# Kernel tuning notes

Measured on AMD Instinct MI355X. Metric: run time of the kernel, lower is better.

## Reference

```python
import jax, jax.numpy as jnp
import numpy as np

N_ITEMS = 100000
N_USERS = 40000
EMB = 100
NNZ_A = 3200000
NNZ_U = 1600000
BATCH = 4096
LAYERS = 3


def setup_inputs() -> dict:
    key = jax.random.key(0)
    ks = jax.random.split(key, 9)
    return {
        "adj_vals": jax.random.uniform(ks[0], (NNZ_A,), dtype=jnp.float32),
        "u_vals": jax.random.uniform(ks[1], (NNZ_U,), dtype=jnp.float32),
        "embedding": jax.random.normal(ks[2], (N_ITEMS, EMB), dtype=jnp.float32),
        "user_embedding": jax.random.normal(ks[3], (N_USERS, EMB), dtype=jnp.float32),
        "adj_rows": jax.random.randint(ks[4], (NNZ_A,), 0, N_ITEMS),
        "adj_cols": jax.random.randint(ks[5], (NNZ_A,), 0, N_ITEMS),
        "u_rows": jax.random.randint(ks[6], (NNZ_U,), 0, N_USERS),
        "u_cols": jax.random.randint(ks[7], (NNZ_U,), 0, N_ITEMS),
        "user": jax.random.randint(ks[8], (BATCH,), 0, N_USERS),
    }


def spmm(vals, rows, cols, x, n_rows):
    # COO sparse (n_rows x n_cols) @ dense x: gather rows of x by col index,
    # scale by nnz values, scatter-add into output rows.
    return jax.ops.segment_sum(vals[:, None] * x[cols], rows, num_segments=n_rows)


def reference(adj_vals, u_vals, embedding, user_embedding,
              adj_rows, adj_cols, u_rows, u_cols, user):
    # Multi-hop hypergraph propagation with running layer-sum (final = sum of layers 0..L)
    x = embedding
    total = x
    for _ in range(LAYERS):
        x = spmm(adj_vals, adj_rows, adj_cols, x, embedding.shape[0])
        total = total + x
    # ishyper branch: user embeddings = (u_adj @ summed item embeddings)[user]
    user_all = spmm(u_vals, u_rows, u_cols, total, user_embedding.shape[0])
    return total, user_all[user]
```

## Files before the change

kernel.cpp:

```cpp
#include <hip/hip_runtime.h>
#include <stdint.h>

#define EMB 100
#define HW 50
#define HW2 25
#define V4_PER_ROW 25
#define BSHIFT 8
#define NBMAX 1024
#define TP 256
#define EP 32

#define SCAN_T 256
#define SCAN_E 32

static __device__ __forceinline__ uint32_t pack_bf16(float a, float b) {
    uint32_t ua = __float_as_uint(a);
    uint32_t ub = __float_as_uint(b);
    ua = (ua + 0x7FFFu + ((ua >> 16) & 1u)) >> 16;
    ub = (ub + 0x7FFFu + ((ub >> 16) & 1u)) >> 16;
    return ua | (ub << 16);
}
static __device__ __forceinline__ float bflo(uint32_t p) { return __uint_as_float(p << 16); }
static __device__ __forceinline__ float bfhi(uint32_t p) { return __uint_as_float(p & 0xFFFF0000u); }

__global__ void convert_bf16(const float2* __restrict__ x, uint32_t* __restrict__ xbf, int nwords) {
    for (int i = blockIdx.x * blockDim.x + threadIdx.x; i < nwords; i += gridDim.x * blockDim.x) {
        float2 v = x[i];
        xbf[i] = pack_bf16(v.x, v.y);
    }
}

__global__ void map_build(const int* __restrict__ user, uint32_t* __restrict__ map, int batch) {
    int i = blockIdx.x * blockDim.x + threadIdx.x;
    if (i < batch) atomicMin(&map[user[i]], (uint32_t)i);
}

__global__ __launch_bounds__(TP) void pass1_count(
    const int* __restrict__ ra, int na, const int* __restrict__ ru, int nu,
    const uint32_t* __restrict__ map, int* __restrict__ countsT,
    int nblk, int nbA, int nbTot)
{
    __shared__ int lc[NBMAX];
    const int blk = blockIdx.x;
    for (int i = threadIdx.x; i < nbTot; i += TP) lc[i] = 0;
    __syncthreads();
    const int base = blk * (TP * EP);
    const int n = na + nu;
    for (int i = 0; i < EP; ++i) {
        int e = base + i * TP + threadIdx.x;
        int b = -1;
        if (e < na) {
            b = __builtin_nontemporal_load(ra + e) >> BSHIFT;
        } else if (e < n) {
            int r = __builtin_nontemporal_load(ru + (e - na));
            if (map[r] != 0xFFFFFFFFu) b = nbA + (r >> BSHIFT);
        }
        if (b >= 0) atomicAdd(&lc[b], 1);
    }
    __syncthreads();
    for (int i = threadIdx.x; i < nbTot; i += TP)
        countsT[(size_t)i * nblk + blk] = lc[i];
}

__global__ void scan_blocks(const int* __restrict__ in, int* __restrict__ out,
                            int* __restrict__ sums, int n) {
    __shared__ int smem[SCAN_T];
    const int b = blockIdx.x, tid = threadIdx.x;
    const int base = b * SCAN_T * SCAN_E + tid * SCAN_E;
    int loc[SCAN_E];
    int s = 0;
    for (int i = 0; i < SCAN_E; ++i) {
        int idx = base + i;
        int v = (idx < n) ? in[idx] : 0;
        loc[i] = s; s += v;
    }
    smem[tid] = s; __syncthreads();
    for (int off = 1; off < SCAN_T; off <<= 1) {
        int v = (tid >= off) ? smem[tid - off] : 0;
        __syncthreads();
        smem[tid] += v;
        __syncthreads();
    }
    int pre = (tid == 0) ? 0 : smem[tid - 1];
    if (tid == SCAN_T - 1) sums[b] = smem[tid];
    for (int i = 0; i < SCAN_E; ++i) {
        int idx = base + i;
        if (idx < n) out[idx] = pre + loc[i];
    }
}

__global__ void scan_mid(int* __restrict__ sums, int nb, int* __restrict__ total_out) {
    __shared__ int sh[256];
    const int t = threadIdx.x;
    int v = (t < nb) ? sums[t] : 0;
    sh[t] = v; __syncthreads();
    for (int off = 1; off < 256; off <<= 1) {
        int u = (t >= off) ? sh[t - off] : 0;
        __syncthreads();
        sh[t] += u;
        __syncthreads();
    }
    if (t < nb) sums[t] = sh[t];
    if (t == 255) *total_out = sh[255];
}

__global__ void scan_fixup(int* __restrict__ out, const int* __restrict__ sums, int n) {
    const int b = blockIdx.x;
    if (b == 0) return;
    const int add = sums[b - 1];
    const int base = b * SCAN_T * SCAN_E + threadIdx.x * SCAN_E;
    for (int i = 0; i < SCAN_E; ++i) {
        int idx = base + i;
        if (idx < n) out[idx] += add;
    }
}

__global__ void extract_bases(const int* __restrict__ scanned, int nblk, int nbTot,
                              const int* __restrict__ total, int* __restrict__ bases,
                              int* __restrict__ rpA_end, int nnzA, int* __restrict__ rpU_end) {
    int t = blockIdx.x * blockDim.x + threadIdx.x;
    if (t < nbTot) bases[t] = scanned[(size_t)t * nblk];
    if (t == 0) {
        int tot = *total;
        bases[nbTot] = tot;
        *rpA_end = nnzA;
        *rpU_end = tot - nnzA;
    }
}

__global__ __launch_bounds__(TP) void pass2_scatter(
    const float* __restrict__ va, const int* __restrict__ ra, const int* __restrict__ ia, int na,
    const float* __restrict__ vu, const int* __restrict__ ru, const int* __restrict__ iu, int nu,
    const uint32_t* __restrict__ map, const int* __restrict__ scanned,
    uint2* __restrict__ tmp, int nblk, int nbA, int nbTot)
{
    __shared__ int cur[NBMAX];
    const int blk = blockIdx.x;
    for (int i = threadIdx.x; i < nbTot; i += TP)
        cur[i] = scanned[(size_t)i * nblk + blk];
    __syncthreads();
    const int base = blk * (TP * EP);
    const int n = na + nu;
    for (int i = 0; i < EP; ++i) {
        int e = base + i * TP + threadIdx.x;
        if (e < na) {
            int r = __builtin_nontemporal_load(ra + e);
            int p = atomicAdd(&cur[r >> BSHIFT], 1);
            uint32_t key = ((uint32_t)(r & 255) << 17) | (uint32_t)__builtin_nontemporal_load(ia + e);
            tmp[p] = make_uint2(key, (uint32_t)__float_as_uint(__builtin_nontemporal_load(va + e)));
        } else if (e < n) {
            int k = e - na;
            int r = __builtin_nontemporal_load(ru + k);
            if (map[r] == 0xFFFFFFFFu) continue;
            int p = atomicAdd(&cur[nbA + (r >> BSHIFT)], 1);
            uint32_t key = ((uint32_t)(r & 255) << 17) | (uint32_t)__builtin_nontemporal_load(iu + k);
            tmp[p] = make_uint2(key, (uint32_t)__float_as_uint(__builtin_nontemporal_load(vu + k)));
        }
    }
}

__global__ __launch_bounds__(1024) void bucket_sort(const uint2* __restrict__ tmp,
                                                    const int* __restrict__ bases,
                                                    uint32_t* __restrict__ pk,
                                                    int* __restrict__ rpA, int* __restrict__ rpU,
                                                    int nbA, int nnzA, int nItems, int nUsers) {
    __shared__ int h[256];
    __shared__ int cur[256];
    const int t = threadIdx.x;
    const int b = blockIdx.x;
    const int lo = bases[b], hi = bases[b + 1];
    const bool isU = (b >= nbA);
    const int rowbase = (isU ? (b - nbA) : b) << BSHIFT;

    if (t < 256) h[t] = 0;
    __syncthreads();
    for (int i = lo + t; i < hi; i += 1024)
        atomicAdd(&h[tmp[i].x >> 17], 1);
    __syncthreads();
    int cnt = (t < 256) ? h[t] : 0;
    for (int off = 1; off < 256; off <<= 1) {
        int u = (t < 256 && t >= off) ? h[t - off] : 0;
        __syncthreads();
        if (t < 256) h[t] += u;
        __syncthreads();
    }
    if (t < 256) {
        int gpos = lo + h[t] - cnt;
        int row = rowbase + t;
        if (isU) { if (row < nUsers) rpU[row] = gpos - nnzA; }
        else     { if (row < nItems) rpA[row] = gpos; }
        cur[t] = gpos;
    }
    __syncthreads();
    for (int i = lo + t; i < hi; i += 1024) {
        uint2 e = tmp[i];
        int rl = (int)(e.x >> 17);
        uint32_t col = e.x & 0x1FFFFu;
        int p = atomicAdd(&cur[rl], 1);
        float v = __uint_as_float(e.y);
        uint32_t q = (uint32_t)(v * 32767.0f + 0.5f);
        if (q > 32767u) q = 32767u;
        pk[p] = (col << 15) | q;
    }
}

#define DECODE(w, v, c) { v = (float)((w) & 0x7FFFu) * (1.0f/32767.0f); c = (int)((w) >> 15); }

#define FMA2(vv, pp) { a0 = fmaf((vv), bflo((pp).x), a0); a1 = fmaf((vv), bfhi((pp).x), a1); \
                       a2 = fmaf((vv), bflo((pp).y), a2); a3 = fmaf((vv), bfhi((pp).y), a3); }

__global__ __launch_bounds__(256) void spmm_pk(
    const uint32_t* __restrict__ pk, const int* __restrict__ rowptr,
    const uint2* __restrict__ xbf2, uint2* __restrict__ outbf2,
    const float4* __restrict__ emb4, const uint2* __restrict__ x1bf2,
    const uint2* __restrict__ x2bf2, float4* __restrict__ total4,
    uint2* __restrict__ totbf2, int nrows)
{
    const int wid = (blockIdx.x * blockDim.x + threadIdx.x) >> 6;
    const int lane = threadIdx.x & 63;
    if (wid >= nrows) return;
    const int half = lane >> 5;
    const int l = lane & 31;
    const int start = rowptr[wid], end = rowptr[wid + 1];
    float a0 = 0.f, a1 = 0.f, a2 = 0.f, a3 = 0.f;
    for (int base = start; base < end; base += 64) {
        const int nc = min(64, end - base);
        uint32_t w = 0;
        if (lane < nc) w = __builtin_nontemporal_load(pk + base + lane);
        float myv; int myc;
        DECODE(w, myv, myc);
        int t = 0;
        for (; t + 8 <= nc; t += 8) {
            float v0 = __shfl(myv, t + half),     v1 = __shfl(myv, t + 2 + half);
            float v2 = __shfl(myv, t + 4 + half), v3 = __shfl(myv, t + 6 + half);
            int   c0 = __shfl(myc, t + half),     c1 = __shfl(myc, t + 2 + half);
            int   c2 = __shfl(myc, t + 4 + half), c3 = __shfl(myc, t + 6 + half);
            uint2 p0 = make_uint2(0u,0u), p1 = make_uint2(0u,0u);
            uint2 p2 = make_uint2(0u,0u), p3 = make_uint2(0u,0u);
            if (l < HW2) {
                p0 = xbf2[(size_t)c0 * HW2 + l];
                p1 = xbf2[(size_t)c1 * HW2 + l];
                p2 = xbf2[(size_t)c2 * HW2 + l];
                p3 = xbf2[(size_t)c3 * HW2 + l];
            }
            FMA2(v0, p0); FMA2(v1, p1); FMA2(v2, p2); FMA2(v3, p3);
        }
        for (; t < nc; t += 2) {
            int tt = min(t + half, nc - 1);
            float v0 = __shfl(myv, tt);
            int   c0 = __shfl(myc, tt);
            if (t + half >= nc) v0 = 0.f;
            uint2 p0 = make_uint2(0u,0u);
            if (l < HW2) p0 = xbf2[(size_t)c0 * HW2 + l];
            FMA2(v0, p0);
        }
    }
    a0 += __shfl_xor(a0, 32); a1 += __shfl_xor(a1, 32);
    a2 += __shfl_xor(a2, 32); a3 += __shfl_xor(a3, 32);
    if (lane < HW2) {
        const size_t widx = (size_t)wid * HW2 + lane;
        if (outbf2) {
            outbf2[widx] = make_uint2(pack_bf16(a0, a1), pack_bf16(a2, a3));
        } else {
            float4 e = emb4[widx];
            uint2 w1 = x1bf2[widx], w2 = x2bf2[widx];
            float t0 = e.x + bflo(w1.x) + bflo(w2.x) + a0;
            float t1 = e.y + bfhi(w1.x) + bfhi(w2.x) + a1;
            float t2 = e.z + bflo(w1.y) + bflo(w2.y) + a2;
            float t3 = e.w + bfhi(w1.y) + bfhi(w2.y) + a3;
            total4[widx] = make_float4(t0, t1, t2, t3);
            totbf2[widx] = make_uint2(pack_bf16(t0, t1), pack_bf16(t2, t3));
        }
    }
}

__global__ __launch_bounds__(256) void spmm_batch_pk(
    const uint32_t* __restrict__ pk, const int* __restrict__ rowptr,
    const int* __restrict__ user, const uint2* __restrict__ xbf2,
    float4* __restrict__ out4, int batch)
{
    const int wid = (blockIdx.x * blockDim.x + threadIdx.x) >> 6;
    const int lane = threadIdx.x & 63;
    if (wid >= batch) return;
    const int half = lane >> 5;
    const int l = lane & 31;
    const int row = user[wid];
    const int start = rowptr[row], end = rowptr[row + 1];
    float a0 = 0.f, a1 = 0.f, a2 = 0.f, a3 = 0.f;
    for (int base = start; base < end; base += 64) {
        const int nc = min(64, end - base);
        uint32_t w = 0;
        if (lane < nc) w = __builtin_nontemporal_load(pk + base + lane);
        float myv; int myc;
        DECODE(w, myv, myc);
        int t = 0;
        for (; t + 8 <= nc; t += 8) {
            float v0 = __shfl(myv, t + half),     v1 = __shfl(myv, t + 2 + half);
            float v2 = __shfl(myv, t + 4 + half), v3 = __shfl(myv, t + 6 + half);
            int   c0 = __shfl(myc, t + half),     c1 = __shfl(myc, t + 2 + half);
            int   c2 = __shfl(myc, t + 4 + half), c3 = __shfl(myc, t + 6 + half);
            uint2 p0 = make_uint2(0u,0u), p1 = make_uint2(0u,0u);
            uint2 p2 = make_uint2(0u,0u), p3 = make_uint2(0u,0u);
            if (l < HW2) {
                p0 = xbf2[(size_t)c0 * HW2 + l];
                p1 = xbf2[(size_t)c1 * HW2 + l];
                p2 = xbf2[(size_t)c2 * HW2 + l];
                p3 = xbf2[(size_t)c3 * HW2 + l];
            }
            FMA2(v0, p0); FMA2(v1, p1); FMA2(v2, p2); FMA2(v3, p3);
        }
        for (; t < nc; t += 2) {
            int tt = min(t + half, nc - 1);
            float v0 = __shfl(myv, tt);
            int   c0 = __shfl(myc, tt);
            if (t + half >= nc) v0 = 0.f;
            uint2 p0 = make_uint2(0u,0u);
            if (l < HW2) p0 = xbf2[(size_t)c0 * HW2 + l];
            FMA2(v0, p0);
        }
    }
    a0 += __shfl_xor(a0, 32); a1 += __shfl_xor(a1, 32);
    a2 += __shfl_xor(a2, 32); a3 += __shfl_xor(a3, 32);
    if (lane < HW2) out4[(size_t)wid * HW2 + lane] = make_float4(a0, a1, a2, a3);
}

__global__ void spmm_scatter(const float* __restrict__ vals, const int* __restrict__ rows,
                             const int* __restrict__ cols, const float* __restrict__ x,
                             float* __restrict__ out, int nnz) {
    long long t = (long long)blockIdx.x * blockDim.x + threadIdx.x;
    int e = (int)(t / V4_PER_ROW);
    int c = (int)(t % V4_PER_ROW);
    if (e >= nnz) return;
    int col = cols[e]; int row = rows[e]; float v = vals[e];
    const float4 g = *(const float4*)(x + (size_t)col * EMB + c * 4);
    float* o = out + (size_t)row * EMB + c * 4;
    atomicAdd(o + 0, v * g.x); atomicAdd(o + 1, v * g.y);
    atomicAdd(o + 2, v * g.z); atomicAdd(o + 3, v * g.w);
}
__global__ void add_inplace(float* __restrict__ acc, const float* __restrict__ x, int n4) {
    int i = blockIdx.x * blockDim.x + threadIdx.x;
    if (i < n4) {
        float4 a = ((const float4*)acc)[i];
        const float4 b = ((const float4*)x)[i];
        a.x += b.x; a.y += b.y; a.z += b.z; a.w += b.w;
        ((float4*)acc)[i] = a;
    }
}
__global__ void gather_rows(const float* __restrict__ src, const int* __restrict__ idx,
                            float* __restrict__ out, int nrows) {
    int t = blockIdx.x * blockDim.x + threadIdx.x;
    int r = t / V4_PER_ROW, c = t % V4_PER_ROW;
    if (r >= nrows) return;
    int s = idx[r];
    *(float4*)(out + (size_t)r * EMB + c * 4) = *(const float4*)(src + (size_t)s * EMB + c * 4);
}

static inline size_t align256(size_t x) { return (x + 255) & ~(size_t)255; }

extern "C" void kernel_launch(void* const* d_in, const int* in_sizes, int n_in,
                              void* d_out, int out_size, void* d_ws, size_t ws_size,
                              hipStream_t stream) {
    const float* adj_vals  = (const float*)d_in[0];
    const float* u_vals    = (const float*)d_in[1];
    const float* embedding = (const float*)d_in[2];
    const int*   adj_rows  = (const int*)d_in[4];
    const int*   adj_cols  = (const int*)d_in[5];
    const int*   u_rows    = (const int*)d_in[6];
    const int*   u_cols    = (const int*)d_in[7];
    const int*   user      = (const int*)d_in[8];

    const int NNZ_A   = in_sizes[0];
    const int NNZ_U   = in_sizes[1];
    const int N_ITEMS = in_sizes[2] / EMB;
    const int N_USERS = in_sizes[3] / EMB;
    const int BATCH   = in_sizes[8];

    const int NB_A = (N_ITEMS + 255) >> BSHIFT;
    const int NB_U = (N_USERS + 255) >> BSHIFT;
    const int NB_TOT = NB_A + NB_U;

    const int NNZ_T = NNZ_A + NNZ_U;
    const int nblk = (NNZ_T + TP * EP - 1) / (TP * EP);
    const long long nScan = (long long)NB_TOT * nblk;
    const int nsb = (int)((nScan + SCAN_T * SCAN_E - 1) / (SCAN_T * SCAN_E));

    float* total    = (float*)d_out;
    float* out_user = total + (size_t)N_ITEMS * EMB;

    const size_t rowWords = (size_t)N_ITEMS * HW;

    size_t off = 0;
    char* ws = (char*)d_ws;
    #define WS_ALLOC(name, bytes) char* name = ws + off; off += align256(bytes)
    WS_ALLOC(p_r0,      2 * rowWords * 4);
    WS_ALLOC(p_ebf,     rowWords * 4);
    WS_ALLOC(p_pk,      (size_t)NNZ_T * 4);
    WS_ALLOC(p_rpA,     ((size_t)N_ITEMS + 1) * 4);
    WS_ALLOC(p_rpU,     ((size_t)N_USERS + 1) * 4);
    WS_ALLOC(p_map,     (size_t)N_USERS * 4);
    WS_ALLOC(p_countsT, (size_t)nScan * 4);
    WS_ALLOC(p_sums,    256 * 4);
    WS_ALLOC(p_total,   4);
    WS_ALLOC(p_bases,   ((size_t)NB_TOT + 1) * 4);
    #undef WS_ALLOC
    const size_t tmpBytes = (size_t)NNZ_T * 8;

    if (ws_size >= off && tmpBytes <= 2 * rowWords * 4 && NB_TOT <= NBMAX && nsb <= 256
        && N_ITEMS <= (1 << 17) && N_USERS <= (1 << 17)) {
        uint32_t* x1bf  = (uint32_t*)p_r0;
        uint32_t* x2bf  = (uint32_t*)(p_r0 + rowWords * 4);
        uint2*    tmp   = (uint2*)p_r0;
        uint32_t* embbf = (uint32_t*)p_ebf;
        uint32_t* totbf = (uint32_t*)p_ebf;
        uint32_t* pk    = (uint32_t*)p_pk;
        int* rpA = (int*)p_rpA;
        int* rpU = (int*)p_rpU;
        uint32_t* map = (uint32_t*)p_map;
        int* countsT = (int*)p_countsT;
        int* sums    = (int*)p_sums;
        int* totalN  = (int*)p_total;
        int* bases   = (int*)p_bases;

        hipMemsetAsync(map, 0xFF, (size_t)N_USERS * 4, stream);
        map_build<<<(BATCH + 255) / 256, 256, 0, stream>>>(user, map, BATCH);

        convert_bf16<<<2048, 256, 0, stream>>>((const float2*)embedding, embbf, (int)rowWords);

        pass1_count<<<nblk, TP, 0, stream>>>(adj_rows, NNZ_A, u_rows, NNZ_U, map,
                                             countsT, nblk, NB_A, NB_TOT);
        scan_blocks<<<nsb, SCAN_T, 0, stream>>>(countsT, countsT, sums, (int)nScan);
        scan_mid<<<1, 256, 0, stream>>>(sums, nsb, totalN);
        scan_fixup<<<nsb, SCAN_T, 0, stream>>>(countsT, sums, (int)nScan);
        extract_bases<<<(NB_TOT + 255) / 256, 256, 0, stream>>>(countsT, nblk, NB_TOT, totalN,
                                                                bases, rpA + N_ITEMS, NNZ_A,
                                                                rpU + N_USERS);
        pass2_scatter<<<nblk, TP, 0, stream>>>(adj_vals, adj_rows, adj_cols, NNZ_A,
                                               u_vals, u_rows, u_cols, NNZ_U,
                                               map, countsT, tmp, nblk, NB_A, NB_TOT);
        bucket_sort<<<NB_TOT, 1024, 0, stream>>>(tmp, bases, pk, rpA, rpU,
                                                 NB_A, NNZ_A, N_ITEMS, N_USERS);

        const int gridA = (N_ITEMS + 3) / 4;
        spmm_pk<<<gridA, 256, 0, stream>>>(pk, rpA, (const uint2*)embbf, (uint2*)x1bf,
                                           nullptr, nullptr, nullptr, nullptr, nullptr, N_ITEMS);
        spmm_pk<<<gridA, 256, 0, stream>>>(pk, rpA, (const uint2*)x1bf, (uint2*)x2bf,
                                           nullptr, nullptr, nullptr, nullptr, nullptr, N_ITEMS);
        spmm_pk<<<gridA, 256, 0, stream>>>(pk, rpA, (const uint2*)x2bf, nullptr,
                                           (const float4*)embedding, (const uint2*)x1bf,
                                           (const uint2*)x2bf, (float4*)total,
                                           (uint2*)totbf, N_ITEMS);
        spmm_batch_pk<<<(BATCH + 3) / 4, 256, 0, stream>>>(pk + NNZ_A, rpU, user,
                                                           (const uint2*)totbf,
                                                           (float4*)out_user, BATCH);
    } else {
        const size_t itemBytes = (size_t)N_ITEMS * EMB * sizeof(float);
        float* buf0 = (float*)d_ws;
        float* buf1 = buf0 + (size_t)N_ITEMS * EMB;
        float* user_all = buf1;
        const size_t userBytes = (size_t)N_USERS * EMB * sizeof(float);

        hipMemcpyAsync(total, embedding, itemBytes, hipMemcpyDeviceToDevice, stream);
        const int blkA = (NNZ_A * V4_PER_ROW + 255) / 256;
        const int blkU = (NNZ_U * V4_PER_ROW + 255) / 256;
        const int n4 = N_ITEMS * EMB / 4;
        const int blkAdd = (n4 + 255) / 256;

        hipMemsetAsync(buf0, 0, itemBytes, stream);
        spmm_scatter<<<blkA, 256, 0, stream>>>(adj_vals, adj_rows, adj_cols, embedding, buf0, NNZ_A);
        add_inplace<<<blkAdd, 256, 0, stream>>>(total, buf0, n4);
        hipMemsetAsync(buf1, 0, itemBytes, stream);
        spmm_scatter<<<blkA, 256, 0, stream>>>(adj_vals, adj_rows, adj_cols, buf0, buf1, NNZ_A);
        add_inplace<<<blkAdd, 256, 0, stream>>>(total, buf1, n4);
        hipMemsetAsync(buf0, 0, itemBytes, stream);
        spmm_scatter<<<blkA, 256, 0, stream>>>(adj_vals, adj_rows, adj_cols, buf1, buf0, NNZ_A);
        add_inplace<<<blkAdd, 256, 0, stream>>>(total, buf0, n4);
        hipMemsetAsync(user_all, 0, userBytes, stream);
        spmm_scatter<<<blkU, 256, 0, stream>>>(u_vals, u_rows, u_cols, total, user_all, NNZ_U);
        gather_rows<<<(BATCH * V4_PER_ROW + 255) / 256, 256, 0, stream>>>(user_all, user, out_user, BATCH);
    }
}
```

Baseline: 569.6 us.

## Split bf16 embeddings into column slices so SpMM gathers fit in cache

Stores the bf16 embedding and intermediate layers as 7 column slices of 16 features (32 bytes per row each). The SpMM then runs one grid dimension per slice, with 8 nonzeros handled per wavefront step. The aim is to shrink the working set each slice pass gathers from (about 3.2 MB per slice instead of 20 MB) so random gathers hit L2/infinity cache more often. In exchange, the row pointers and packed nonzeros are re-read 7 times, the padding wastes a few lanes in the last slice, and each gather becomes a small 32-byte access.

Result: slower. 1.095 ms (+92.2%).

```diff
diff --git a/kernel.cpp b/kernel.cpp
--- a/kernel.cpp
+++ b/kernel.cpp
@@ -2,7 +2,6 @@
 #include <stdint.h>
 
 #define EMB 100
-#define HW 50
 #define HW2 25
 #define V4_PER_ROW 25
 #define BSHIFT 8
@@ -10,6 +9,9 @@
 #define TP 256
 #define EP 32
 
+#define NSLICE 7
+#define SLW 8
+
 #define SCAN_T 256
 #define SCAN_E 32
 
@@ -23,11 +25,18 @@
 static __device__ __forceinline__ float bflo(uint32_t p) { return __uint_as_float(p << 16); }
 static __device__ __forceinline__ float bfhi(uint32_t p) { return __uint_as_float(p & 0xFFFF0000u); }
 
-__global__ void convert_bf16(const float2* __restrict__ x, uint32_t* __restrict__ xbf, int nwords) {
-    for (int i = blockIdx.x * blockDim.x + threadIdx.x; i < nwords; i += gridDim.x * blockDim.x) {
-        float2 v = x[i];
-        xbf[i] = pack_bf16(v.x, v.y);
-    }
+__global__ void convert_sl(const float2* __restrict__ x, uint32_t* __restrict__ xs, int nrows) {
+    const int slice = blockIdx.y;
+    const int tid = blockIdx.x * blockDim.x + threadIdx.x;
+    if (tid >= nrows * SLW) return;
+    const int row = tid >> 3, j = tid & 7;
+    const int d0 = slice * 16 + j * 2;
+    uint32_t v = 0;
+    if (d0 < EMB) {
+        float2 f = x[(size_t)row * 50 + slice * SLW + j];
+        v = pack_bf16(f.x, f.y);
+    }
+    xs[(size_t)slice * nrows * SLW + tid] = v;
 }
 
 __global__ void map_build(const int* __restrict__ user, uint32_t* __restrict__ map, int batch) {
@@ -206,73 +215,61 @@
 
 #define DECODE(w, v, c) { v = (float)((w) & 0x7FFFu) * (1.0f/32767.0f); c = (int)((w) >> 15); }
 
-#define FMA2(vv, pp) { a0 = fmaf((vv), bflo((pp).x), a0); a1 = fmaf((vv), bfhi((pp).x), a1); \
-                       a2 = fmaf((vv), bflo((pp).y), a2); a3 = fmaf((vv), bfhi((pp).y), a3); }
-
-__global__ __launch_bounds__(256) void spmm_pk(
+__global__ __launch_bounds__(256) void spmm_sl(
     const uint32_t* __restrict__ pk, const int* __restrict__ rowptr,
-    const uint2* __restrict__ xbf2, uint2* __restrict__ outbf2,
-    const float4* __restrict__ emb4, const uint2* __restrict__ x1bf2,
-    const uint2* __restrict__ x2bf2, float4* __restrict__ total4,
-    uint2* __restrict__ totbf2, int nrows)
+    const uint32_t* __restrict__ xs,
+    uint32_t* __restrict__ outs,
+    const float2* __restrict__ emb2,
+    const uint32_t* __restrict__ x1s, const uint32_t* __restrict__ x2s,
+    float2* __restrict__ total2, uint32_t* __restrict__ totu,
+    int nrows)
 {
-    const int wid = (blockIdx.x * blockDim.x + threadIdx.x) >> 6;
+    const int slice = blockIdx.y;
+    const int row = blockIdx.x * 4 + (threadIdx.x >> 6);
+    if (row >= nrows) return;
     const int lane = threadIdx.x & 63;
-    if (wid >= nrows) return;
-    const int half = lane >> 5;
-    const int l = lane & 31;
-    const int start = rowptr[wid], end = rowptr[wid + 1];
-    float a0 = 0.f, a1 = 0.f, a2 = 0.f, a3 = 0.f;
+    const int g = lane >> 3, j = lane & 7;
+    const size_t sb = (size_t)slice * nrows * SLW;
+    const int start = rowptr[row], end = rowptr[row + 1];
+    float a0 = 0.f, a1 = 0.f;
     for (int base = start; base < end; base += 64) {
         const int nc = min(64, end - base);
         uint32_t w = 0;
         if (lane < nc) w = __builtin_nontemporal_load(pk + base + lane);
         float myv; int myc;
         DECODE(w, myv, myc);
-        int t = 0;
-        for (; t + 8 <= nc; t += 8) {
-            float v0 = __shfl(myv, t + half),     v1 = __shfl(myv, t + 2 + half);
-            float v2 = __shfl(myv, t + 4 + half), v3 = __shfl(myv, t + 6 + half);
-            int   c0 = __shfl(myc, t + half),     c1 = __shfl(myc, t + 2 + half);
-            int   c2 = __shfl(myc, t + 4 + half), c3 = __shfl(myc, t + 6 + half);
-            uint2 p0 = make_uint2(0u,0u), p1 = make_uint2(0u,0u);
-            uint2 p2 = make_uint2(0u,0u), p3 = make_uint2(0u,0u);
-            if (l < HW2) {
-                p0 = xbf2[(size_t)c0 * HW2 + l];
-                p1 = xbf2[(size_t)c1 * HW2 + l];
-                p2 = xbf2[(size_t)c2 * HW2 + l];
-                p3 = xbf2[(size_t)c3 * HW2 + l];
+        for (int t = 0; t < nc; t += 8) {
+            float v = __shfl(myv, t + g);
+            int   c = __shfl(myc, t + g);
+            uint32_t p = xs[sb + (size_t)c * SLW + j];
+            a0 = fmaf(v, bflo(p), a0);
+            a1 = fmaf(v, bfhi(p), a1);
+        }
+    }
+    a0 += __shfl_xor(a0, 8);  a1 += __shfl_xor(a1, 8);
+    a0 += __shfl_xor(a0, 16); a1 += __shfl_xor(a1, 16);
+    a0 += __shfl_xor(a0, 32); a1 += __shfl_xor(a1, 32);
+    if (lane < SLW) {
+        if (outs) {
+            outs[sb + (size_t)row * SLW + lane] = pack_bf16(a0, a1);
+        } else {
+            const int d0 = slice * 16 + lane * 2;
+            if (d0 < EMB) {
+                const size_t ri = (size_t)row * 50 + slice * SLW + lane;
+                float2 e = emb2[ri];
+                uint32_t w1 = x1s[sb + (size_t)row * SLW + lane];
+                uint32_t w2 = x2s[sb + (size_t)row * SLW + lane];
+                float t0 = e.x + bflo(w1) + bflo(w2) + a0;
+                float t1 = e.y + bfhi(w1) + bfhi(w2) + a1;
+                total2[ri] = make_float2(t0, t1);
+                totu[ri] = pack_bf16(t0, t1);
             }
-            FMA2(v0, p0); FMA2(v1, p1); FMA2(v2, p2); FMA2(v3, p3);
-        }
-        for (; t < nc; t += 2) {
-            int tt = min(t + half, nc - 1);
-            float v0 = __shfl(myv, tt);
-            int   c0 = __shfl(myc, tt);
-            if (t + half >= nc) v0 = 0.f;
-            uint2 p0 = make_uint2(0u,0u);
-            if (l < HW2) p0 = xbf2[(size_t)c0 * HW2 + l];
-            FMA2(v0, p0);
-        }
-    }
-    a0 += __shfl_xor(a0, 32); a1 += __shfl_xor(a1, 32);
-    a2 += __shfl_xor(a2, 32); a3 += __shfl_xor(a3, 32);
-    if (lane < HW2) {
-        const size_t widx = (size_t)wid * HW2 + lane;
-        if (outbf2) {
-            outbf2[widx] = make_uint2(pack_bf16(a0, a1), pack_bf16(a2, a3));
-        } else {
-            float4 e = emb4[widx];
-            uint2 w1 = x1bf2[widx], w2 = x2bf2[widx];
-            float t0 = e.x + bflo(w1.x) + bflo(w2.x) + a0;
-            float t1 = e.y + bfhi(w1.x) + bfhi(w2.x) + a1;
-            float t2 = e.z + bflo(w1.y) + bflo(w2.y) + a2;
-            float t3 = e.w + bfhi(w1.y) + bfhi(w2.y) + a3;
-            total4[widx] = make_float4(t0, t1, t2, t3);
-            totbf2[widx] = make_uint2(pack_bf16(t0, t1), pack_bf16(t2, t3));
-        }
-    }
-}
+        }
+    }
+}
+
+#define FMA2(vv, pp) { a0 = fmaf((vv), bflo((pp).x), a0); a1 = fmaf((vv), bfhi((pp).x), a1); \
+                       a2 = fmaf((vv), bflo((pp).y), a2); a3 = fmaf((vv), bfhi((pp).y), a3); }
 
 __global__ __launch_bounds__(256) void spmm_batch_pk(
     const uint32_t* __restrict__ pk, const int* __restrict__ rowptr,
@@ -387,13 +384,13 @@
     float* total    = (float*)d_out;
     float* out_user = total + (size_t)N_ITEMS * EMB;
 
-    const size_t rowWords = (size_t)N_ITEMS * HW;
+    const size_t sliceWords = (size_t)N_ITEMS * NSLICE * SLW;
 
     size_t off = 0;
     char* ws = (char*)d_ws;
     #define WS_ALLOC(name, bytes) char* name = ws + off; off += align256(bytes)
-    WS_ALLOC(p_r0,      2 * rowWords * 4);
-    WS_ALLOC(p_ebf,     rowWords * 4);
+    WS_ALLOC(p_x12,     2 * sliceWords * 4);
+    WS_ALLOC(p_ebf,     sliceWords * 4);
     WS_ALLOC(p_pk,      (size_t)NNZ_T * 4);
     WS_ALLOC(p_rpA,     ((size_t)N_ITEMS + 1) * 4);
     WS_ALLOC(p_rpU,     ((size_t)N_USERS + 1) * 4);
@@ -405,13 +402,13 @@
     #undef WS_ALLOC
     const size_t tmpBytes = (size_t)NNZ_T * 8;
 
-    if (ws_size >= off && tmpBytes <= 2 * rowWords * 4 && NB_TOT <= NBMAX && nsb <= 256
+    if (ws_size >= off && tmpBytes <= 2 * sliceWords * 4 && NB_TOT <= NBMAX && nsb <= 256
         && N_ITEMS <= (1 << 17) && N_USERS <= (1 << 17)) {
-        uint32_t* x1bf  = (uint32_t*)p_r0;
-        uint32_t* x2bf  = (uint32_t*)(p_r0 + rowWords * 4);
-        uint2*    tmp   = (uint2*)p_r0;
-        uint32_t* embbf = (uint32_t*)p_ebf;
-        uint32_t* totbf = (uint32_t*)p_ebf;
+        uint32_t* x1s   = (uint32_t*)p_x12;
+        uint32_t* x2s   = x1s + sliceWords;
+        uint2*    tmp   = (uint2*)p_x12;
+        uint32_t* embs  = (uint32_t*)p_ebf;
+        uint32_t* totu  = (uint32_t*)p_ebf;
         uint32_t* pk    = (uint32_t*)p_pk;
         int* rpA = (int*)p_rpA;
         int* rpU = (int*)p_rpU;
@@ -424,7 +421,10 @@
         hipMemsetAsync(map, 0xFF, (size_t)N_USERS * 4, stream);
         map_build<<<(BATCH + 255) / 256, 256, 0, stream>>>(user, map, BATCH);
 
-        convert_bf16<<<2048, 256, 0, stream>>>((const float2*)embedding, embbf, (int)rowWords);
+        {
+            dim3 g((N_ITEMS * SLW + 255) / 256, NSLICE);
+            convert_sl<<<g, 256, 0, stream>>>((const float2*)embedding, embs, N_ITEMS);
+        }
 
         pass1_count<<<nblk, TP, 0, stream>>>(adj_rows, NNZ_A, u_rows, NNZ_U, map,
                                              countsT, nblk, NB_A, NB_TOT);
@@ -440,17 +440,17 @@
         bucket_sort<<<NB_TOT, 1024, 0, stream>>>(tmp, bases, pk, rpA, rpU,
                                                  NB_A, NNZ_A, N_ITEMS, N_USERS);
 
-        const int gridA = (N_ITEMS + 3) / 4;
-        spmm_pk<<<gridA, 256, 0, stream>>>(pk, rpA, (const uint2*)embbf, (uint2*)x1bf,
+        const int bps = (N_ITEMS + 3) / 4;
+        dim3 gridA(bps, NSLICE);
+        spmm_sl<<<gridA, 256, 0, stream>>>(pk, rpA, embs, x1s,
                                            nullptr, nullptr, nullptr, nullptr, nullptr, N_ITEMS);
-        spmm_pk<<<gridA, 256, 0, stream>>>(pk, rpA, (const uint2*)x1bf, (uint2*)x2bf,
+        spmm_sl<<<gridA, 256, 0, stream>>>(pk, rpA, x1s, x2s,
                                            nullptr, nullptr, nullptr, nullptr, nullptr, N_ITEMS);
-        spmm_pk<<<gridA, 256, 0, stream>>>(pk, rpA, (const uint2*)x2bf, nullptr,
-                                           (const float4*)embedding, (const uint2*)x1bf,
-                                           (const uint2*)x2bf, (float4*)total,
-                                           (uint2*)totbf, N_ITEMS);
+        spmm_sl<<<gridA, 256, 0, stream>>>(pk, rpA, x2s, nullptr,
+                                           (const float2*)embedding, x1s, x2s,
+                                           (float2*)total, totu, N_ITEMS);
         spmm_batch_pk<<<(BATCH + 3) / 4, 256, 0, stream>>>(pk + NNZ_A, rpU, user,
-                                                           (const uint2*)totbf,
+                                                           (const uint2*)totu,
                                                            (float4*)out_user, BATCH);
     } else {
         const size_t itemBytes = (size_t)N_ITEMS * EMB * sizeof(float);
```
